# Kernel tuning notes

Measured on AMD Instinct MI355X. Metric: run time of the kernel, lower is better.

The kernel has to match this reference:

```python
import jax, jax.numpy as jnp
import numpy as np

L, H, P, R = 4096, 1024, 512, 16
DT_MIN, DT_MAX = 1e-3, 1e-1

def setup_inputs() -> dict:
    key = jax.random.key(0)
    ks = jax.random.split(key, 16)
    return {
        "input_sequence": jax.random.normal(ks[0], (L, H), jnp.float32),
        # HiPPO-like eigenvalues: negative real part, spread imaginary part
        "Lambda_re": (-0.5 * jax.random.uniform(ks[1], (P,), jnp.float32) - 1e-2),
        "Lambda_im": 3.0 * jax.random.normal(ks[2], (P,), jnp.float32),
        "B_re": jax.random.normal(ks[3], (P, H), jnp.float32) / np.float32(np.sqrt(H)),
        "B_im": jax.random.normal(ks[4], (P, H), jnp.float32) / np.float32(np.sqrt(H)),
        "C_re": jax.random.normal(ks[5], (H, 2 * P), jnp.float32) / np.float32(np.sqrt(2 * P)),
        "C_im": jax.random.normal(ks[6], (H, 2 * P), jnp.float32) / np.float32(np.sqrt(2 * P)),
        "E_re": 0.01 * jax.random.normal(ks[7], (P, R), jnp.float32),
        "E_im": 0.01 * jax.random.normal(ks[8], (P, R), jnp.float32),
        "F_re": 0.01 * jax.random.normal(ks[9], (R, P), jnp.float32),
        "F_im": 0.01 * jax.random.normal(ks[10], (R, P), jnp.float32),
        "D": jax.random.normal(ks[11], (H,), jnp.float32),
        "log_step": np.float32(np.log(DT_MIN)) + jax.random.uniform(ks[12], (P,), jnp.float32) * np.float32(np.log(DT_MAX) - np.log(DT_MIN)),
        "Delta_t_diag": 0.01 * jax.random.normal(ks[13], (L, R), jnp.float32),
    }

def _scan_op(q_i, q_j):
    # diagonal linear recurrence combine: x_j = A_j * x_i + b_j
    A_i, b_i = q_i
    A_j, b_j = q_j
    return (A_j * A_i, A_j * b_i + b_j)

def reference(input_sequence, Lambda_re, Lambda_im, B_re, B_im, C_re, C_im,
              E_re, E_im, F_re, F_im, D, log_step, Delta_t_diag):
    # clip_eigs=True: enforce left-half-plane
    Lam = jnp.clip(Lambda_re, None, -1e-4) + 1j * Lambda_im            # (P,)
    step = jnp.exp(log_step)                                           # (P,)  step_rescale=1.0
    # zoh discretization
    Lambda_bar = jnp.exp(Lam * step)                                   # (P,)
    B_tilde = B_re + 1j * B_im                                         # (P,H)
    B_bar = ((Lambda_bar - 1.0) / Lam)[:, None] * B_tilde              # (P,H)
    # Lambda extension: diag(E @ diag(d_l) @ F)[p] = sum_r E[p,r] d_l[r] F[r,p]
    E = E_re + 1j * E_im                                               # (P,R)
    F = F_re + 1j * F_im                                               # (R,P)
    EF = E.T * F                                                       # (R,P)
    ext = Delta_t_diag.astype(EF.dtype) @ EF                           # (L,P)
    Lambda_elements = Lambda_bar[None, :] + ext                        # (L,P)
    Bu_elements = input_sequence.astype(B_bar.dtype) @ B_bar.T         # (L,P)
    _, xs_f = jax.lax.associative_scan(_scan_op, (Lambda_elements, Bu_elements))
    _, xs_b = jax.lax.associative_scan(_scan_op, (Lambda_elements, Bu_elements), reverse=True)
    xs = jnp.concatenate((xs_f, xs_b), axis=-1)                        # (L,2P) bidirectional
    C_tilde = C_re + 1j * C_im                                         # (H,2P)
    ys = 2.0 * (xs @ C_tilde.T).real                                   # conj_sym=True -> 2*Re
    return ys + D * input_sequence                                     # feedthrough
```

## Files before the change

kernel.cpp:

```cpp
#include <hip/hip_runtime.h>

#define LL 4096
#define HH 1024
#define PP 512
#define RR 16
#define CH 128
#define CL 32

typedef _Float16 f16x8 __attribute__((ext_vector_type(8)));
typedef float f32x4 __attribute__((ext_vector_type(4)));
typedef unsigned short u16;
typedef unsigned int u32;

#define MF16(a, b, c) __builtin_amdgcn_mfma_f32_16x16x32_f16(a, b, c, 0, 0, 0)

__device__ __forceinline__ u16 h16(float x) {
  _Float16 h = (_Float16)x;
  return __builtin_bit_cast(u16, h);
}
__device__ __forceinline__ float f16f(u16 v) {
  return (float)__builtin_bit_cast(_Float16, v);
}

__global__ void precompute_kernel(const float* __restrict__ Lre, const float* __restrict__ Lim,
                                  const float* __restrict__ lst,
                                  const float* __restrict__ Ere, const float* __restrict__ Eim,
                                  const float* __restrict__ Fre, const float* __restrict__ Fim,
                                  float* __restrict__ Lbr, float* __restrict__ Lbi,
                                  float* __restrict__ cfr, float* __restrict__ cfi,
                                  float* __restrict__ EFr, float* __restrict__ EFi)
{
  int p = blockIdx.x * blockDim.x + threadIdx.x;
  if (p >= PP) return;
  float lre = fminf(Lre[p], -1e-4f);
  float lim = Lim[p];
  float st  = expf(lst[p]);
  float er  = expf(lre * st);
  float s, c;
  sincosf(lim * st, &s, &c);
  float lbr = er * c, lbi = er * s;
  Lbr[p] = lbr; Lbi[p] = lbi;
  float den = lre * lre + lim * lim;
  float nr  = lbr - 1.0f;
  cfr[p] = (nr * lre + lbi * lim) / den;
  cfi[p] = (lbi * lre - nr * lim) / den;
  for (int r = 0; r < RR; ++r) {
    float e_r = Ere[p * RR + r], e_i = Eim[p * RR + r];
    float f_r = Fre[r * PP + p], f_i = Fim[r * PP + p];
    EFr[r * PP + p] = e_r * f_r - e_i * f_i;
    EFi[r * PP + p] = e_r * f_i + e_i * f_r;
  }
}

__global__ __launch_bounds__(256) void prep2_kernel(
    const float* __restrict__ Bre, const float* __restrict__ Bim,
    const float* __restrict__ cfr, const float* __restrict__ cfi,
    const float* __restrict__ Cre, const float* __restrict__ Cim,
    const float* __restrict__ Dt, const float* __restrict__ EFr,
    const float* __restrict__ EFi,
    u16* __restrict__ B1, u32* __restrict__ B2, u32* __restrict__ LE)
{
  int g = blockIdx.x, t = threadIdx.x;
  if (g < 512) {
    int base = (g * 256 + t) * 4;
    int p = base >> 10, col = base & 1023;
    float cr = cfr[p], ci = cfi[p];
    float4 br = *(const float4*)&Bre[base];
    float4 bi = *(const float4*)&Bim[base];
    ushort4 rp, ip;
    rp.x = h16(cr*br.x - ci*bi.x); ip.x = h16(cr*bi.x + ci*br.x);
    rp.y = h16(cr*br.y - ci*bi.y); ip.y = h16(cr*bi.y + ci*br.y);
    rp.z = h16(cr*br.z - ci*bi.z); ip.z = h16(cr*bi.z + ci*br.z);
    rp.w = h16(cr*br.w - ci*bi.w); ip.w = h16(cr*bi.w + ci*br.w);
    *(ushort4*)&B1[(size_t)(2 * p) * 1024 + col] = rp;
    *(ushort4*)&B1[(size_t)(2 * p + 1) * 1024 + col] = ip;
  } else if (g < 1536) {
    int base = ((g - 512) * 256 + t) * 4;
    float4 a = *(const float4*)&Cre[base];
    float4 b = *(const float4*)&Cim[base];
    uint4 o;
    o.x = (u32)h16(a.x) | ((u32)h16(-b.x) << 16);
    o.y = (u32)h16(a.y) | ((u32)h16(-b.y) << 16);
    o.z = (u32)h16(a.z) | ((u32)h16(-b.z) << 16);
    o.w = (u32)h16(a.w) | ((u32)h16(-b.w) << 16);
    *(uint4*)&B2[base] = o;
  } else {
    int gid = (g - 1536) * 256 + t;
    int l  = gid >> 7;
    int pq = (gid & 127) << 2;
    float4 ar = {0.f, 0.f, 0.f, 0.f};
    float4 ai = {0.f, 0.f, 0.f, 0.f};
#pragma unroll
    for (int r = 0; r < RR; ++r) {
      float d = Dt[l * RR + r];
      float4 er = *(const float4*)&EFr[r * PP + pq];
      float4 ei = *(const float4*)&EFi[r * PP + pq];
      ar.x = fmaf(d, er.x, ar.x); ar.y = fmaf(d, er.y, ar.y);
      ar.z = fmaf(d, er.z, ar.z); ar.w = fmaf(d, er.w, ar.w);
      ai.x = fmaf(d, ei.x, ai.x); ai.y = fmaf(d, ei.y, ai.y);
      ai.z = fmaf(d, ei.z, ai.z); ai.w = fmaf(d, ei.w, ai.w);
    }
    uint4 o;
    o.x = (u32)h16(ar.x) | ((u32)h16(ai.x) << 16);
    o.y = (u32)h16(ar.y) | ((u32)h16(ai.y) << 16);
    o.z = (u32)h16(ar.z) | ((u32)h16(ai.z) << 16);
    o.w = (u32)h16(ar.w) | ((u32)h16(ai.w) << 16);
    *(uint4*)&LE[(size_t)l * PP + pq] = o;
  }
}

template<int EPI, bool ACVT>
__global__ __launch_bounds__(256) void gemm_k(
    const void* __restrict__ Asrc, const u16* __restrict__ Bsrc, int Kp,
    void* __restrict__ outv, const float* __restrict__ Dv,
    const float* __restrict__ Uep)
{
  __shared__ __align__(16) uint4 lds[2 * 16 * 64];
  int bid = blockIdx.x;
  int n0 = ((bid & 7) * 2 + ((bid >> 3) & 1)) * 64;
  int m0 = (bid >> 4) * 64;
  int t = threadIdx.x, lane = t & 63, w = t >> 6;
  int wr = w >> 1, wc = w & 1;
  int rl = lane & 15, kg = lane >> 4;
  int crow = t >> 2, cch = t & 3;
  int NT = Kp / 64;

  const float* Af = (const float*)Asrc;
  const u16*   Ah = (const u16*)Asrc;

  f32x4 acc[2][2];
  acc[0][0] = acc[0][1] = acc[1][0] = acc[1][1] = (f32x4){0.f, 0.f, 0.f, 0.f};

  struct Frags { uint4 a[2]; uint4 b[2]; };
  auto LOAD = [&](int kt) -> Frags {
    Frags f;
    if constexpr (ACVT) {
      const float* p = Af + (size_t)(m0 + crow) * Kp + kt * 64 + cch * 16;
#pragma unroll
      for (int j = 0; j < 2; ++j) {
        float4 a = *(const float4*)(p + j * 8), b = *(const float4*)(p + j * 8 + 4);
        f16x8 r;
        r[0] = (_Float16)a.x; r[1] = (_Float16)a.y; r[2] = (_Float16)a.z; r[3] = (_Float16)a.w;
        r[4] = (_Float16)b.x; r[5] = (_Float16)b.y; r[6] = (_Float16)b.z; r[7] = (_Float16)b.w;
        f.a[j] = __builtin_bit_cast(uint4, r);
      }
    } else {
      const u16* p = Ah + (size_t)(m0 + crow) * Kp + kt * 64 + cch * 16;
      f.a[0] = *(const uint4*)p;
      f.a[1] = *(const uint4*)(p + 8);
    }
    const u16* q = Bsrc + (size_t)(n0 + crow) * Kp + kt * 64 + cch * 16;
    f.b[0] = *(const uint4*)q;
    f.b[1] = *(const uint4*)(q + 8);
    return f;
  };
  auto WRITE = [&](int buf, const Frags& f) {
#pragma unroll
    for (int j = 0; j < 2; ++j) {
      int kq = cch * 2 + j;
      int c = kq & 3;
      int slot = c * 16 + ((crow & 15) ^ (c * 2));
      int segA = (crow >> 4) * 2 + (kq >> 2);
      lds[buf * 1024 + segA * 64 + slot] = f.a[j];
      lds[buf * 1024 + (8 + segA) * 64 + slot] = f.b[j];
    }
  };

  Frags nxt, far;
  WRITE(0, LOAD(0));
  nxt = LOAD(1);
  __syncthreads();

  for (int kt = 0; kt < NT; ++kt) {
    int c = kt & 1;
    if (kt + 2 < NT) far = LOAD(kt + 2);
    int rslot = kg * 16 + (rl ^ (kg * 2));
    f16x8 af[2][2], bf[2][2];
#pragma unroll
    for (int m = 0; m < 2; ++m)
#pragma unroll
      for (int ks = 0; ks < 2; ++ks) {
        int segA = (wr * 2 + m) * 2 + ks;
        int segB = 8 + (wc * 2 + m) * 2 + ks;
        af[m][ks] = __builtin_bit_cast(f16x8, lds[c * 1024 + segA * 64 + rslot]);
        bf[m][ks] = __builtin_bit_cast(f16x8, lds[c * 1024 + segB * 64 + rslot]);
      }
#pragma unroll
    for (int ks = 0; ks < 2; ++ks)
#pragma unroll
      for (int m = 0; m < 2; ++m)
#pragma unroll
        for (int n = 0; n < 2; ++n)
          acc[m][n] = MF16(af[m][ks], bf[n][ks], acc[m][n]);
    if (kt + 1 < NT) WRITE(c ^ 1, nxt);
    nxt = far;
    __syncthreads();
  }

  float* Stg = (float*)lds;
#pragma unroll
  for (int m = 0; m < 2; ++m)
#pragma unroll
    for (int n = 0; n < 2; ++n)
#pragma unroll
      for (int j = 0; j < 4; ++j)
        Stg[(wr * 32 + m * 16 + kg * 4 + j) * 68 + wc * 32 + n * 16 + rl] = acc[m][n][j];
  __syncthreads();
  int col4 = (t & 15) * 4, prow = t >> 4;
#pragma unroll
  for (int i = 0; i < 4; ++i) {
    int r = prow + 16 * i;
    float4 v = *(const float4*)&Stg[r * 68 + col4];
    if constexpr (EPI == 2) {
      uint2 pk;
      pk.x = (u32)h16(v.x) | ((u32)h16(v.y) << 16);
      pk.y = (u32)h16(v.z) | ((u32)h16(v.w) << 16);
      u32* outp = (u32*)outv;
      *(uint2*)&outp[(size_t)(m0 + r) * 512 + (n0 + col4) / 2] = pk;
    } else {
      float* out = (float*)outv;
      size_t ob = (size_t)(m0 + r) * 1024 + n0 + col4;
      if constexpr (EPI == 1) {
        float4 u4 = *(const float4*)&Uep[ob];
        float4 dv = *(const float4*)&Dv[n0 + col4];
        v.x = 2.f * v.x + dv.x * u4.x; v.y = 2.f * v.y + dv.y * u4.y;
        v.z = 2.f * v.z + dv.z * u4.z; v.w = 2.f * v.w + dv.w * u4.w;
      }
      *(float4*)&out[ob] = v;
    }
  }
}

__global__ __launch_bounds__(256) void scan_agg_kernel(
    const float* __restrict__ Lbr, const float* __restrict__ Lbi,
    const u32* __restrict__ LE, const u32* __restrict__ P2,
    float* __restrict__ aggAr, float* __restrict__ aggAi,
    float* __restrict__ aggBr, float* __restrict__ aggBi)
{
  int tid = blockIdx.x * 256 + threadIdx.x;
  int p   = tid & (PP - 1);
  int c   = (tid >> 9) & (CH - 1);
  int dir = tid >> 16;
  float lbr = Lbr[p], lbi = Lbi[p];
  float Ar = 1.f, Ai = 0.f, br = 0.f, bi = 0.f;
  int base = c * CL;
#pragma unroll
  for (int g = 0; g < CL / 8; ++g) {
    float ar8[8], ai8[8], br8[8], bi8[8];
#pragma unroll
    for (int u = 0; u < 8; ++u) {
      int l = base + g * 8 + u;
      int phys = dir ? (LL - 1 - l) : l;
      u32 v = LE[(size_t)phys * PP + p];
      u32 bv = P2[(size_t)phys * PP + p];
      ar8[u] = lbr + f16f((u16)(v & 0xffff));
      ai8[u] = lbi + f16f((u16)(v >> 16));
      br8[u] = f16f((u16)(bv & 0xffff));
      bi8[u] = f16f((u16)(bv >> 16));
    }
#pragma unroll
    for (int u = 0; u < 8; ++u) {
      float nAr = ar8[u] * Ar - ai8[u] * Ai;
      float nAi = ar8[u] * Ai + ai8[u] * Ar;
      float nbr = fmaf(ar8[u], br, fmaf(-ai8[u], bi, br8[u]));
      float nbi = fmaf(ar8[u], bi, fmaf( ai8[u], br, bi8[u]));
      Ar = nAr; Ai = nAi; br = nbr; bi = nbi;
    }
  }
  aggAr[tid] = Ar; aggAi[tid] = Ai; aggBr[tid] = br; aggBi[tid] = bi;
}

__global__ __launch_bounds__(256) void scan_carry_kernel(
    const float* __restrict__ aggAr, const float* __restrict__ aggAi,
    const float* __restrict__ aggBr, const float* __restrict__ aggBi,
    float* __restrict__ carR, float* __restrict__ carI)
{
  int tid = blockIdx.x * 256 + threadIdx.x;
  int p   = tid & (PP - 1);
  int dir = tid >> 9;
  float xr = 0.f, xi = 0.f;
  for (int c = 0; c < CH; ++c) {
    int idx = (dir * CH + c) * PP + p;
    carR[idx] = xr; carI[idx] = xi;
    float ar = aggAr[idx], ai = aggAi[idx];
    float br = aggBr[idx], bi = aggBi[idx];
    float nr = fmaf(ar, xr, fmaf(-ai, xi, br));
    float ni = fmaf(ar, xi, fmaf( ai, xr, bi));
    xr = nr; xi = ni;
  }
}

__global__ __launch_bounds__(256) void scan_apply_kernel(
    const float* __restrict__ Lbr, const float* __restrict__ Lbi,
    const u32* __restrict__ LE, const u32* __restrict__ P2,
    const float* __restrict__ carR, const float* __restrict__ carI,
    u32* __restrict__ A2)
{
  int tid = blockIdx.x * 256 + threadIdx.x;
  int p   = tid & (PP - 1);
  int c   = (tid >> 9) & (CH - 1);
  int dir = tid >> 16;
  float lbr = Lbr[p], lbi = Lbi[p];
  float xr = carR[tid], xi = carI[tid];
  int base = c * CL;
  int cofs = dir * PP + p;
#pragma unroll
  for (int g = 0; g < CL / 8; ++g) {
    float ar8[8], ai8[8], br8[8], bi8[8];
#pragma unroll
    for (int u = 0; u < 8; ++u) {
      int l = base + g * 8 + u;
      int phys = dir ? (LL - 1 - l) : l;
      u32 v = LE[(size_t)phys * PP + p];
      u32 bv = P2[(size_t)phys * PP + p];
      ar8[u] = lbr + f16f((u16)(v & 0xffff));
      ai8[u] = lbi + f16f((u16)(v >> 16));
      br8[u] = f16f((u16)(bv & 0xffff));
      bi8[u] = f16f((u16)(bv >> 16));
    }
#pragma unroll
    for (int u = 0; u < 8; ++u) {
      float nr = fmaf(ar8[u], xr, fmaf(-ai8[u], xi, br8[u]));
      float ni = fmaf(ar8[u], xi, fmaf( ai8[u], xr, bi8[u]));
      xr = nr; xi = ni;
      int l = base + g * 8 + u;
      int phys = dir ? (LL - 1 - l) : l;
      A2[(size_t)phys * 1024 + cofs] = (u32)h16(xr) | ((u32)h16(xi) << 16);
    }
  }
}

extern "C" void kernel_launch(void* const* d_in, const int* in_sizes, int n_in,
                              void* d_out, int out_size, void* d_ws, size_t ws_size,
                              hipStream_t stream)
{
  const float* U   = (const float*)d_in[0];
  const float* Lre = (const float*)d_in[1];
  const float* Lim = (const float*)d_in[2];
  const float* Bre = (const float*)d_in[3];
  const float* Bim = (const float*)d_in[4];
  const float* Cre = (const float*)d_in[5];
  const float* Cim = (const float*)d_in[6];
  const float* Ere = (const float*)d_in[7];
  const float* Eim = (const float*)d_in[8];
  const float* Fre = (const float*)d_in[9];
  const float* Fim = (const float*)d_in[10];
  const float* Dv  = (const float*)d_in[11];
  const float* lst = (const float*)d_in[12];
  const float* Dt  = (const float*)d_in[13];
  float* Y = (float*)d_out;

  char* wsb = (char*)d_ws;
  size_t o = 0;
  auto alloc = [&](size_t bytes) -> char* {
    char* r = wsb + o; o += (bytes + 255) & ~(size_t)255; return r;
  };
  float* Lbr = (float*)alloc(PP * 4);
  float* Lbi = (float*)alloc(PP * 4);
  float* cfr = (float*)alloc(PP * 4);
  float* cfi = (float*)alloc(PP * 4);
  float* EFr = (float*)alloc((size_t)RR * PP * 4);
  float* EFi = (float*)alloc((size_t)RR * PP * 4);
  u16* B1 = (u16*)alloc((size_t)1024 * 1024 * 2);
  u32* B2 = (u32*)alloc((size_t)1024 * 1024 * 4);
  u32* LE = (u32*)alloc((size_t)LL * PP * 4);
  u32* P2 = (u32*)alloc((size_t)LL * PP * 4);
  u32* A2 = (u32*)alloc((size_t)LL * 1024 * 4);
  const int NAGG = 2 * CH * PP;
  float* aggAr = (float*)alloc((size_t)NAGG * 4);
  float* aggAi = (float*)alloc((size_t)NAGG * 4);
  float* aggBr = (float*)alloc((size_t)NAGG * 4);
  float* aggBi = (float*)alloc((size_t)NAGG * 4);
  float* carR  = (float*)alloc((size_t)NAGG * 4);
  float* carI  = (float*)alloc((size_t)NAGG * 4);

  precompute_kernel<<<2, 256, 0, stream>>>(Lre, Lim, lst, Ere, Eim, Fre, Fim,
                                           Lbr, Lbi, cfr, cfi, EFr, EFi);
  prep2_kernel<<<3584, 256, 0, stream>>>(Bre, Bim, cfr, cfi, Cre, Cim,
                                         Dt, EFr, EFi, B1, B2, LE);
  gemm_k<2, true><<<1024, 256, 0, stream>>>(U, B1, 1024, P2, nullptr, nullptr);
  scan_agg_kernel<<<2 * CH * PP / 256, 256, 0, stream>>>(Lbr, Lbi, LE, P2,
                                                         aggAr, aggAi, aggBr, aggBi);
  scan_carry_kernel<<<4, 256, 0, stream>>>(aggAr, aggAi, aggBr, aggBi, carR, carI);
  scan_apply_kernel<<<2 * CH * PP / 256, 256, 0, stream>>>(Lbr, Lbi, LE, P2, carR, carI, A2);
  gemm_k<1, false><<<1024, 256, 0, stream>>>(A2, (const u16*)B2, 2048, Y, Dv, U);
}
```

Before: 114.5 us.

## Enlarge GEMM tiles to 128x128 with K-step 32 and direct register epilogue

Both GEMMs now use 128x128 output tiles per block with a 32-wide K step, so each wave computes a 4x4 grid of MFMA tiles instead of 2x2. This raises arithmetic intensity per LDS and global load, and cuts the grid from 1024 to 256 blocks. The LDS-staged epilogue is replaced by direct stores from accumulators, with lane shuffles packing fp16 pairs. The costs are fewer blocks than CUs (256 on an MI355X), higher register pressure, twice as many K iterations and barriers, and less coalesced scattered stores.

```diff
diff --git a/kernel.cpp b/kernel.cpp
--- a/kernel.cpp
+++ b/kernel.cpp
@@ -117,25 +117,28 @@
 {
   __shared__ __align__(16) uint4 lds[2 * 16 * 64];
   int bid = blockIdx.x;
-  int n0 = ((bid & 7) * 2 + ((bid >> 3) & 1)) * 64;
-  int m0 = (bid >> 4) * 64;
+  int n0 = (bid & 7) * 128;
+  int m0 = (bid >> 3) * 128;
   int t = threadIdx.x, lane = t & 63, w = t >> 6;
   int wr = w >> 1, wc = w & 1;
   int rl = lane & 15, kg = lane >> 4;
-  int crow = t >> 2, cch = t & 3;
-  int NT = Kp / 64;
+  int srow = t >> 1, shalf = t & 1;
+  int NT = Kp / 32;
 
   const float* Af = (const float*)Asrc;
   const u16*   Ah = (const u16*)Asrc;
 
-  f32x4 acc[2][2];
-  acc[0][0] = acc[0][1] = acc[1][0] = acc[1][1] = (f32x4){0.f, 0.f, 0.f, 0.f};
+  f32x4 acc[4][4];
+#pragma unroll
+  for (int m = 0; m < 4; ++m)
+#pragma unroll
+    for (int n = 0; n < 4; ++n) acc[m][n] = (f32x4){0.f, 0.f, 0.f, 0.f};
 
   struct Frags { uint4 a[2]; uint4 b[2]; };
   auto LOAD = [&](int kt) -> Frags {
     Frags f;
     if constexpr (ACVT) {
-      const float* p = Af + (size_t)(m0 + crow) * Kp + kt * 64 + cch * 16;
+      const float* p = Af + (size_t)(m0 + srow) * Kp + kt * 32 + shalf * 16;
 #pragma unroll
       for (int j = 0; j < 2; ++j) {
         float4 a = *(const float4*)(p + j * 8), b = *(const float4*)(p + j * 8 + 4);
@@ -145,11 +148,11 @@
         f.a[j] = __builtin_bit_cast(uint4, r);
       }
     } else {
-      const u16* p = Ah + (size_t)(m0 + crow) * Kp + kt * 64 + cch * 16;
+      const u16* p = Ah + (size_t)(m0 + srow) * Kp + kt * 32 + shalf * 16;
       f.a[0] = *(const uint4*)p;
       f.a[1] = *(const uint4*)(p + 8);
     }
-    const u16* q = Bsrc + (size_t)(n0 + crow) * Kp + kt * 64 + cch * 16;
+    const u16* q = Bsrc + (size_t)(n0 + srow) * Kp + kt * 32 + shalf * 16;
     f.b[0] = *(const uint4*)q;
     f.b[1] = *(const uint4*)(q + 8);
     return f;
@@ -157,12 +160,11 @@
   auto WRITE = [&](int buf, const Frags& f) {
 #pragma unroll
     for (int j = 0; j < 2; ++j) {
-      int kq = cch * 2 + j;
-      int c = kq & 3;
-      int slot = c * 16 + ((crow & 15) ^ (c * 2));
-      int segA = (crow >> 4) * 2 + (kq >> 2);
-      lds[buf * 1024 + segA * 64 + slot] = f.a[j];
-      lds[buf * 1024 + (8 + segA) * 64 + slot] = f.b[j];
+      int kq = shalf * 2 + j;
+      int slot = kq * 16 + ((srow & 15) ^ (2 * kq));
+      int seg = srow >> 4;
+      lds[buf * 1024 + seg * 64 + slot] = f.a[j];
+      lds[buf * 1024 + (8 + seg) * 64 + slot] = f.b[j];
     }
   };
 
@@ -175,58 +177,53 @@
     int c = kt & 1;
     if (kt + 2 < NT) far = LOAD(kt + 2);
     int rslot = kg * 16 + (rl ^ (kg * 2));
-    f16x8 af[2][2], bf[2][2];
-#pragma unroll
-    for (int m = 0; m < 2; ++m)
-#pragma unroll
-      for (int ks = 0; ks < 2; ++ks) {
-        int segA = (wr * 2 + m) * 2 + ks;
-        int segB = 8 + (wc * 2 + m) * 2 + ks;
-        af[m][ks] = __builtin_bit_cast(f16x8, lds[c * 1024 + segA * 64 + rslot]);
-        bf[m][ks] = __builtin_bit_cast(f16x8, lds[c * 1024 + segB * 64 + rslot]);
-      }
-#pragma unroll
-    for (int ks = 0; ks < 2; ++ks)
-#pragma unroll
-      for (int m = 0; m < 2; ++m)
-#pragma unroll
-        for (int n = 0; n < 2; ++n)
-          acc[m][n] = MF16(af[m][ks], bf[n][ks], acc[m][n]);
+    f16x8 af[4], bf[4];
+#pragma unroll
+    for (int m = 0; m < 4; ++m)
+      af[m] = __builtin_bit_cast(f16x8, lds[c * 1024 + (wr * 4 + m) * 64 + rslot]);
+#pragma unroll
+    for (int n = 0; n < 4; ++n)
+      bf[n] = __builtin_bit_cast(f16x8, lds[c * 1024 + (8 + wc * 4 + n) * 64 + rslot]);
+#pragma unroll
+    for (int m = 0; m < 4; ++m)
+#pragma unroll
+      for (int n = 0; n < 4; ++n)
+        acc[m][n] = MF16(af[m], bf[n], acc[m][n]);
     if (kt + 1 < NT) WRITE(c ^ 1, nxt);
     nxt = far;
     __syncthreads();
   }
 
-  float* Stg = (float*)lds;
-#pragma unroll
-  for (int m = 0; m < 2; ++m)
-#pragma unroll
-    for (int n = 0; n < 2; ++n)
-#pragma unroll
-      for (int j = 0; j < 4; ++j)
-        Stg[(wr * 32 + m * 16 + kg * 4 + j) * 68 + wc * 32 + n * 16 + rl] = acc[m][n][j];
-  __syncthreads();
-  int col4 = (t & 15) * 4, prow = t >> 4;
-#pragma unroll
-  for (int i = 0; i < 4; ++i) {
-    int r = prow + 16 * i;
-    float4 v = *(const float4*)&Stg[r * 68 + col4];
-    if constexpr (EPI == 2) {
-      uint2 pk;
-      pk.x = (u32)h16(v.x) | ((u32)h16(v.y) << 16);
-      pk.y = (u32)h16(v.z) | ((u32)h16(v.w) << 16);
-      u32* outp = (u32*)outv;
-      *(uint2*)&outp[(size_t)(m0 + r) * 512 + (n0 + col4) / 2] = pk;
-    } else {
-      float* out = (float*)outv;
-      size_t ob = (size_t)(m0 + r) * 1024 + n0 + col4;
-      if constexpr (EPI == 1) {
-        float4 u4 = *(const float4*)&Uep[ob];
-        float4 dv = *(const float4*)&Dv[n0 + col4];
-        v.x = 2.f * v.x + dv.x * u4.x; v.y = 2.f * v.y + dv.y * u4.y;
-        v.z = 2.f * v.z + dv.z * u4.z; v.w = 2.f * v.w + dv.w * u4.w;
-      }
-      *(float4*)&out[ob] = v;
+  if constexpr (EPI == 1) {
+    float* Y = (float*)outv;
+#pragma unroll
+    for (int n = 0; n < 4; ++n) {
+      int col = n0 + wc * 64 + n * 16 + rl;
+      float dv = Dv[col];
+#pragma unroll
+      for (int m = 0; m < 4; ++m)
+#pragma unroll
+        for (int j = 0; j < 4; ++j) {
+          int row = m0 + wr * 64 + m * 16 + kg * 4 + j;
+          size_t idx = (size_t)row * 1024 + col;
+          Y[idx] = 2.f * acc[m][n][j] + dv * Uep[idx];
+        }
+    }
+  } else {
+    u32* P2 = (u32*)outv;
+#pragma unroll
+    for (int n = 0; n < 4; ++n) {
+      int col = n0 + wc * 64 + n * 16 + rl;
+#pragma unroll
+      for (int m = 0; m < 4; ++m)
+#pragma unroll
+        for (int j = 0; j < 4; ++j) {
+          int row = m0 + wr * 64 + m * 16 + kg * 4 + j;
+          u32 hx = (u32)h16(acc[m][n][j]);
+          u32 px = (u32)__shfl_xor((int)hx, 1);
+          if ((rl & 1) == 0)
+            P2[(size_t)row * 512 + (col >> 1)] = hx | (px << 16);
+        }
     }
   }
 }
@@ -378,10 +375,10 @@
                                            Lbr, Lbi, cfr, cfi, EFr, EFi);
   prep2_kernel<<<3584, 256, 0, stream>>>(Bre, Bim, cfr, cfi, Cre, Cim,
                                          Dt, EFr, EFi, B1, B2, LE);
-  gemm_k<2, true><<<1024, 256, 0, stream>>>(U, B1, 1024, P2, nullptr, nullptr);
+  gemm_k<2, true><<<256, 256, 0, stream>>>(U, B1, 1024, P2, nullptr, nullptr);
   scan_agg_kernel<<<2 * CH * PP / 256, 256, 0, stream>>>(Lbr, Lbi, LE, P2,
                                                          aggAr, aggAi, aggBr, aggBi);
   scan_carry_kernel<<<4, 256, 0, stream>>>(aggAr, aggAi, aggBr, aggBi, carR, carI);
   scan_apply_kernel<<<2 * CH * PP / 256, 256, 0, stream>>>(Lbr, Lbi, LE, P2, carR, carI, A2);
-  gemm_k<1, false><<<1024, 256, 0, stream>>>(A2, (const u16*)B2, 2048, Y, Dv, U);
-}
+  gemm_k<1, false><<<256, 256, 0, stream>>>(A2, (const u16*)B2, 2048, Y, Dv, U);
+}
```

Result: slower. 127.7 us (+11.5%).

## Replace output GEMM with 128x128-tile, 8-wave kernel using register-prefetched double-buffered LDS

Applied to the files above, without the earlier changes.

The final GEMM (L x 2048 complex-packed activations times C) moves to a new kernel with 128x128 output tiles, 512 threads and 256 blocks, replacing 1024 smaller blocks. It stages A and B tiles in swizzled, double-buffered shared memory and prefetches global data two k-steps ahead in registers. The aim is better operand reuse and latency hiding. The cost is fewer blocks on a device with many CUs (256 blocks may underfill the GPU), more registers, and scalar rather than vectorized epilogue stores.

```diff
diff --git a/kernel.cpp b/kernel.cpp
--- a/kernel.cpp
+++ b/kernel.cpp
@@ -231,6 +231,99 @@
   }
 }
 
+__global__ __launch_bounds__(512) void gemm2_k8(
+    const u16* __restrict__ Asrc, const u16* __restrict__ Bsrc,
+    float* __restrict__ Y, const float* __restrict__ Dv,
+    const float* __restrict__ Uep)
+{
+  __shared__ __align__(16) uint4 lds[2 * 32 * 64];
+  const int Kp = 2048, NT = 32;
+  int bid = blockIdx.x;
+  int n0 = (bid & 7) * 128;
+  int m0 = (bid >> 3) * 128;
+  int t = threadIdx.x, lane = t & 63, w = t >> 6;
+  int wr = w >> 2, wc = w & 3;
+  int rl = lane & 15, kg = lane >> 4;
+  int srow = t >> 2, cch = t & 3;
+
+  f32x4 acc[4][2];
+#pragma unroll
+  for (int m = 0; m < 4; ++m)
+#pragma unroll
+    for (int n = 0; n < 2; ++n) acc[m][n] = (f32x4){0.f, 0.f, 0.f, 0.f};
+
+  struct Frags { uint4 a[2]; uint4 b[2]; };
+  auto LOAD = [&](int kt) -> Frags {
+    Frags f;
+    const u16* p = Asrc + (size_t)(m0 + srow) * Kp + kt * 64 + cch * 16;
+    f.a[0] = *(const uint4*)p;
+    f.a[1] = *(const uint4*)(p + 8);
+    const u16* q = Bsrc + (size_t)(n0 + srow) * Kp + kt * 64 + cch * 16;
+    f.b[0] = *(const uint4*)q;
+    f.b[1] = *(const uint4*)(q + 8);
+    return f;
+  };
+  auto WRITE = [&](int buf, const Frags& f) {
+#pragma unroll
+    for (int j = 0; j < 2; ++j) {
+      int kq = cch * 2 + j;
+      int c = kq & 3;
+      int slot = c * 16 + ((srow & 15) ^ (c * 2));
+      int seg = (srow >> 4) * 2 + (kq >> 2);
+      lds[buf * 2048 + seg * 64 + slot] = f.a[j];
+      lds[buf * 2048 + (16 + seg) * 64 + slot] = f.b[j];
+    }
+  };
+
+  Frags nxt, far;
+  WRITE(0, LOAD(0));
+  nxt = LOAD(1);
+  __syncthreads();
+
+  for (int kt = 0; kt < NT; ++kt) {
+    int c = kt & 1;
+    if (kt + 2 < NT) far = LOAD(kt + 2);
+    int rslot = kg * 16 + (rl ^ (kg * 2));
+    f16x8 af[4][2], bf[2][2];
+#pragma unroll
+    for (int m = 0; m < 4; ++m)
+#pragma unroll
+      for (int ks = 0; ks < 2; ++ks)
+        af[m][ks] = __builtin_bit_cast(f16x8,
+            lds[c * 2048 + ((wr * 4 + m) * 2 + ks) * 64 + rslot]);
+#pragma unroll
+    for (int n = 0; n < 2; ++n)
+#pragma unroll
+      for (int ks = 0; ks < 2; ++ks)
+        bf[n][ks] = __builtin_bit_cast(f16x8,
+            lds[c * 2048 + (16 + (wc * 2 + n) * 2 + ks) * 64 + rslot]);
+#pragma unroll
+    for (int ks = 0; ks < 2; ++ks)
+#pragma unroll
+      for (int m = 0; m < 4; ++m)
+#pragma unroll
+        for (int n = 0; n < 2; ++n)
+          acc[m][n] = MF16(af[m][ks], bf[n][ks], acc[m][n]);
+    if (kt + 1 < NT) WRITE(c ^ 1, nxt);
+    nxt = far;
+    __syncthreads();
+  }
+
+#pragma unroll
+  for (int n = 0; n < 2; ++n) {
+    int col = n0 + wc * 32 + n * 16 + rl;
+    float dv = Dv[col];
+#pragma unroll
+    for (int m = 0; m < 4; ++m)
+#pragma unroll
+      for (int j = 0; j < 4; ++j) {
+        int row = m0 + wr * 64 + m * 16 + kg * 4 + j;
+        size_t idx = (size_t)row * 1024 + col;
+        Y[idx] = 2.f * acc[m][n][j] + dv * Uep[idx];
+      }
+  }
+}
+
 __global__ __launch_bounds__(256) void scan_agg_kernel(
     const float* __restrict__ Lbr, const float* __restrict__ Lbi,
     const u32* __restrict__ LE, const u32* __restrict__ P2,
@@ -383,5 +476,5 @@
                                                          aggAr, aggAi, aggBr, aggBi);
   scan_carry_kernel<<<4, 256, 0, stream>>>(aggAr, aggAi, aggBr, aggBi, carR, carI);
   scan_apply_kernel<<<2 * CH * PP / 256, 256, 0, stream>>>(Lbr, Lbi, LE, P2, carR, carI, A2);
-  gemm_k<1, false><<<1024, 256, 0, stream>>>(A2, (const u16*)B2, 2048, Y, Dv, U);
-}
+  gemm2_k8<<<256, 512, 0, stream>>>((const u16*)A2, (const u16*)B2, Y, Dv, U);
+}
```

New measurement: 111.3 us. 2.8% less time.
